# Kernel tuning notes

Measured on AMD Instinct MI355X. Metric: run time of the kernel, lower is better.

Reference implementation:

```python
import jax, jax.numpy as jnp
import numpy as np

TEMPERATURE = 0.07
HARD_K = 10
N, D, NUM_CLASSES = 8192, 256, 128


def setup_inputs() -> dict:
    key = jax.random.key(0)
    kf, kl = jax.random.split(key)
    feats = jax.random.normal(kf, (N, D), dtype=jnp.float32)
    labels = jax.random.randint(kl, (N,), 0, NUM_CLASSES, dtype=jnp.int64)
    return {"feats": feats, "labels": labels}


def _loss(feats, labels):
    n = feats.shape[0]
    # F.normalize(dim=-1) with eps=1e-12
    norm = jnp.maximum(jnp.linalg.norm(feats, axis=-1, keepdims=True), 1e-12)
    z = feats / norm
    sim = (z @ z.T) / TEMPERATURE  # [N, N]

    same = labels[:, None] == labels[None, :]
    eye = jnp.eye(n, dtype=bool)
    same_ns = same & ~eye          # same label, excluding self
    diff = ~same                   # different label

    neg_inf = jnp.float32(-jnp.inf)
    # uniform random positive per row via Gumbel-max over the same-label mask
    g = jax.random.gumbel(jax.random.key(42), (n, n), dtype=jnp.float32)
    pos_idx = jnp.argmax(jnp.where(same_ns, g, neg_inf), axis=1)  # [N]
    pos_logit = jnp.take_along_axis(sim, pos_idx[:, None], axis=1)[:, 0]

    # hard negatives: top-k of sims over different-label columns
    neg_sims = jnp.where(diff, sim, neg_inf)
    hard_vals, _ = jax.lax.top_k(neg_sims, HARD_K)  # [N, K]; exp(-inf)=0 handles rows with <K negatives

    num = jnp.exp(pos_logit)
    den = num + jnp.sum(jnp.exp(hard_vals), axis=1)
    li = -jnp.log(jnp.maximum(num / jnp.maximum(den, 1e-8), 1e-8))

    valid = jnp.any(same_ns, axis=1) & jnp.any(diff, axis=1)
    cnt = jnp.maximum(jnp.sum(valid), 1)
    return jnp.sum(jnp.where(valid, li, 0.0)) / cnt.astype(li.dtype)


def reference(feats, labels):
    return _loss(feats, labels)
```

## Files before the change

### kernel.cpp

```cpp
#include <hip/hip_runtime.h>
#include <cstdint>
#include <math.h>

#define N_     8192
#define D_     256
#define NLBL   128
#define TEMP_INV 14.285714285714286f
#define HARDK  10
#define THETA  0.16f
#define GCAP   256

#define NCHUNK 64
#define CHUNK  (N_ / NCHUNK)
#define TILES  (CHUNK / 32)
#define CSLOT  8
#define NTRI   ((NCHUNK * (NCHUNK + 1)) / 2)

typedef __attribute__((ext_vector_type(8)))  short bf16x8;
typedef __attribute__((ext_vector_type(16))) float f32x16;

__device__ __forceinline__ uint32_t rotl32(uint32_t x, int n) {
  return (x << n) | (x >> (32 - n));
}
__device__ uint32_t tf_bits(uint32_t idx) {
  uint32_t x0 = 0u, x1 = idx;
  const uint32_t k0 = 0u, k1 = 42u;
  const uint32_t k2 = k0 ^ k1 ^ 0x1BD11BDAu;
  x0 += k0; x1 += k1;
#define TFR(r) { x0 += x1; x1 = rotl32(x1, r); x1 ^= x0; }
  TFR(13) TFR(15) TFR(26) TFR(6)
  x0 += k1; x1 += k2 + 1u;
  TFR(17) TFR(29) TFR(16) TFR(24)
  x0 += k2; x1 += k0 + 2u;
  TFR(13) TFR(15) TFR(26) TFR(6)
  x0 += k0; x1 += k1 + 3u;
  TFR(17) TFR(29) TFR(16) TFR(24)
  x0 += k1; x1 += k2 + 4u;
  TFR(13) TFR(15) TFR(26) TFR(6)
  x0 += k2; x1 += k0 + 5u;
#undef TFR
  return x0 ^ x1;
}

__device__ __forceinline__ uint32_t f2bf(float x) {
  uint32_t b = __float_as_uint(x);
  return (b + 0x7FFFu + ((b >> 16) & 1u)) >> 16;
}

__global__ __launch_bounds__(256) void prep_group_kernel(
    const float* __restrict__ feats, const int* __restrict__ labels,
    float* __restrict__ inv_norm, unsigned short* __restrict__ zt,
    uint32_t* __restrict__ mask_g, int* __restrict__ glist, int* __restrict__ cnt_g) {
  __shared__ uint4 tile[16][33];
  __shared__ int lcnt;
  const int tid = threadIdx.x;

  if (blockIdx.x < 512) {
    const int row0 = blockIdx.x * 16;
    const int wv = tid >> 6, l = tid & 63;
#pragma unroll
    for (int rr = 0; rr < 4; ++rr) {
      const int rloc = wv * 4 + rr;
      const int row = row0 + rloc;
      float4 v = ((const float4*)feats)[(size_t)row * 64 + l];
      float ss = v.x * v.x + v.y * v.y + v.z * v.z + v.w * v.w;
#pragma unroll
      for (int o = 32; o; o >>= 1) ss += __shfl_xor(ss, o);
      float inv = 1.0f / fmaxf(sqrtf(ss), 1e-12f);
      if (l == 0) inv_norm[row] = inv;
      uint2 p;
      p.x = f2bf(v.x * inv) | (f2bf(v.y * inv) << 16);
      p.y = f2bf(v.z * inv) | (f2bf(v.w * inv) << 16);
      *(uint2*)((char*)&tile[0][0] + rloc * 528 + l * 8) = p;
    }
    __syncthreads();
#pragma unroll
    for (int it = 0; it < 2; ++it) {
      int idx = it * 256 + tid;
      int c = idx >> 4, r = idx & 15;
      ((uint4*)zt)[(size_t)c * N_ + row0 + r] = tile[r][c];
    }
  } else {
    const int b = blockIdx.x - 512;
    const int lane = tid & 63, wv = tid >> 6;
    if (tid == 0) lcnt = 0;
    __syncthreads();
    for (int it = 0; it < N_; it += 256) {
      int col = it + tid;
      bool pred = (labels[col] == b);
      unsigned long long m = __ballot(pred);
      if (lane == 0) {
        int w0 = (it + wv * 64) >> 5;
        mask_g[b * 256 + w0]     = (uint32_t)m;
        mask_g[b * 256 + w0 + 1] = (uint32_t)(m >> 32);
      }
      if (pred) {
        int p = atomicAdd(&lcnt, 1);
        if (p < GCAP) glist[b * GCAP + p] = col;
      }
    }
    __syncthreads();
    if (tid == 0) cnt_g[b] = lcnt;
  }
}

__device__ __forceinline__ void stage_tile(const unsigned short* zt, char (*AbK)[1024],
                                           int colT, int wid, int l, int kg) {
  const char* base = (const char*)zt + ((size_t)kg * N_ + colT + (l & 31)) * 16;
#pragma unroll
  for (int q = 0; q < 4; ++q) {
    const int kk = wid * 4 + q;
    __builtin_amdgcn_global_load_lds(
        (const __attribute__((address_space(1))) void*)(base + (size_t)kk * (2 * N_ * 16)),
        (__attribute__((address_space(3))) void*)(&AbK[kk][0]), 16, 0, 0);
  }
}

#define INS8(H0,H1,H2,H3,H4,H5,H6,H7,POS,C) \
  { H0 = (POS==0)?(C):H0; H1 = (POS==1)?(C):H1; H2 = (POS==2)?(C):H2; H3 = (POS==3)?(C):H3; \
    H4 = (POS==4)?(C):H4; H5 = (POS==5)?(C):H5; H6 = (POS==6)?(C):H6; H7 = (POS==7)?(C):H7; \
    ++POS; }

__global__ __launch_bounds__(256) void collect_kernel(const unsigned short* __restrict__ zt,
                                                      const int* __restrict__ labels,
                                                      const uint32_t* __restrict__ mask_g,
                                                      float* __restrict__ vals,
                                                      int* __restrict__ counts) {
  __shared__ char Ab[2][16][1024];
  __shared__ float mcell[128 * 8];
  __shared__ int   mcnt[128];

  const int tid = threadIdx.x;
  const int l = tid & 63, wid = tid >> 6;
  const int kg = l >> 5;

  const int bid = (blockIdx.x & 7) * (NTRI / 8) + (blockIdx.x >> 3);

  int rc = 0, rem = bid;
  while (rem >= NCHUNK - rc) { rem -= NCHUNK - rc; ++rc; }
  const int cc = rc + rem;
  const bool offdiag = (cc > rc);

  const int row0 = rc * 128;
  const int col0 = cc * CHUNK;
  const int rowW = row0 + wid * 32 + (l & 31);
  const int lab = labels[rowW];

  if (tid < 128) mcnt[tid] = 0;

  uint32_t mW[TILES];
  {
    uint4 m0 = *(const uint4*)(mask_g + lab * 256 + (col0 >> 5));
    mW[0] = m0.x; mW[1] = m0.y; mW[2] = m0.z; mW[3] = m0.w;
  }

  bf16x8 bf[16];
  {
    const uint4* ztq = (const uint4*)zt;
#pragma unroll
    for (int kk = 0; kk < 16; ++kk)
      bf[kk] = *(const bf16x8*)&ztq[(size_t)(kk * 2 + kg) * N_ + rowW];
  }

  float h0=0,h1=0,h2=0,h3=0,h4=0,h5=0,h6=0,h7=0;
  int pos = 0;
  float* vb = vals + ((size_t)rowW * NCHUNK + cc) * CSLOT;

  stage_tile(zt, Ab[0], col0, wid, l, kg);
  __syncthreads();

  int buf = 0;
#pragma unroll
  for (int t = 0; t < TILES; ++t) {
    if (t + 1 < TILES) stage_tile(zt, Ab[buf ^ 1], col0 + (t + 1) * 32, wid, l, kg);

    f32x16 acc;
#pragma unroll
    for (int r = 0; r < 16; ++r) acc[r] = 0.f;
    __builtin_amdgcn_s_setprio(1);
#pragma unroll
    for (int kk = 0; kk < 16; ++kk) {
      bf16x8 a = *(const bf16x8*)&Ab[buf][kk][l * 16];
      acc = __builtin_amdgcn_mfma_f32_32x32x16_bf16(a, bf[kk], acc, 0, 0, 0);
    }
    __builtin_amdgcn_s_setprio(0);

    const uint32_t wsh = mW[t] >> (kg * 4);
#pragma unroll
    for (int r = 0; r < 16; ++r) {
      const int cpos = (r & 3) + 8 * (r >> 2);
      bool hit = ((((wsh >> cpos) & 1u) == 0u) && (acc[r] > THETA));
      if (__any(hit)) {
        if (hit) {
          INS8(h0,h1,h2,h3,h4,h5,h6,h7, pos, acc[r]);
          if (offdiag) {
            int jc = t * 32 + cpos + 4 * kg;
            int p = atomicAdd(&mcnt[jc], 1);
            if (p < 8) mcell[jc * 8 + p] = acc[r];
          }
        }
      }
    }
    __syncthreads();
    buf ^= 1;
  }

  if (kg == 0) {
    if (pos > 0) vb[0] = h0;  if (pos > 1) vb[1] = h1;
    if (pos > 2) vb[2] = h2;  if (pos > 3) vb[3] = h3;
    if (pos > 4) vb[4] = h4;  if (pos > 5) vb[5] = h5;
    if (pos > 6) vb[6] = h6;  if (pos > 7) vb[7] = h7;
  } else {
    if (pos > 0) vb[7] = h0;  if (pos > 1) vb[6] = h1;
    if (pos > 2) vb[5] = h2;  if (pos > 3) vb[4] = h3;
    if (pos > 4) vb[3] = h4;  if (pos > 5) vb[2] = h5;
    if (pos > 6) vb[1] = h6;  if (pos > 7) vb[0] = h7;
  }
  counts[(rowW * NCHUNK + cc) * 2 + kg] = pos;

  if (offdiag) {
    int jc = tid >> 1, half = tid & 1;
    float4 m = *(float4*)&mcell[jc * 8 + half * 4];
    float* dm = vals + ((size_t)(col0 + jc) * NCHUNK + rc) * CSLOT + half * 4;
    *(float4*)dm = m;
    if (half == 0) {
      counts[((col0 + jc) * NCHUNK + rc) * 2 + 0] = mcnt[jc];
      counts[((col0 + jc) * NCHUNK + rc) * 2 + 1] = 0;
    }
  }
}

__global__ __launch_bounds__(256) void finalize_kernel(
    const float* __restrict__ feats, const int* __restrict__ labels,
    const float* __restrict__ inv_norm,
    const int* __restrict__ glist, const int* __restrict__ cnt_g,
    const int* __restrict__ counts, const float* __restrict__ vals,
    float* __restrict__ li, int* __restrict__ valid) {
  const int row = blockIdx.x * 4 + (threadIdx.x >> 6);
  const int lane = threadIdx.x & 63;
  const int lab = labels[row];
  const int gc = cnt_g[lab];
  const int gn = gc < GCAP ? gc : GCAP;
  const float4* feats4 = (const float4*)feats;

  uint32_t bk = 0u; int bj = -1;
  for (int e = lane; e < gn; e += 64) {
    int j = glist[lab * GCAP + e];
    if (j != row) {
      uint32_t key = tf_bits((uint32_t)row * (uint32_t)N_ + (uint32_t)j) >> 9;
      if (bj < 0 || key > bk || (key == bk && j < bj)) { bk = key; bj = j; }
    }
  }
#pragma unroll
  for (int o = 32; o; o >>= 1) {
    uint32_t ok = __shfl_xor(bk, o);
    int oj = __shfl_xor(bj, o);
    if (oj >= 0 && (bj < 0 || ok > bk || (ok == bk && oj < bj))) { bk = ok; bj = oj; }
  }

  float pc = 0.f;
  if (bj >= 0) {
    float4 a = feats4[(size_t)row * 64 + lane];
    float4 b = feats4[(size_t)bj * 64 + lane];
    float p = a.x * b.x + a.y * b.y + a.z * b.z + a.w * b.w;
#pragma unroll
    for (int o = 32; o; o >>= 1) p += __shfl_xor(p, o);
    pc = p * inv_norm[row] * inv_norm[bj];
  }

  float vv[8];
  int ovf = 0;
#pragma unroll
  for (int q = 0; q < 8; ++q) {
    int s = lane + 64 * q;
    int cell = s >> 3, wi = s & 7;
    int c0 = counts[(row * NCHUNK + cell) * 2 + 0];
    int c1 = counts[(row * NCHUNK + cell) * 2 + 1];
    ovf |= (c0 + c1 > CSLOT) ? 1 : 0;
    float val = vals[(size_t)row * (NCHUNK * CSLOT) + s];
    int c1b = c1 < CSLOT ? c1 : CSLOT;
    bool live = (wi < c0) || (wi >= CSLOT - c1b);
    vv[q] = live ? val : -INFINITY;
  }

  float num = expf(pc * TEMP_INV);
  float den = num;
  int got = 0;
#pragma unroll 1
  for (int it = 0; it < HARDK; ++it) {
    float lm = fmaxf(fmaxf(fmaxf(vv[0], vv[1]), fmaxf(vv[2], vv[3])),
                     fmaxf(fmaxf(vv[4], vv[5]), fmaxf(vv[6], vv[7])));
    float wm = lm;
#pragma unroll
    for (int o = 32; o; o >>= 1) wm = fmaxf(wm, __shfl_xor(wm, o));
    if (wm < -1e37f) break;
    den += expf(wm * TEMP_INV);
    ++got;
    unsigned long long b = __ballot(lm == wm);
    int fl = __ffsll((long long)b) - 1;
    if (lane == fl) {
      if      (vv[0] == wm) vv[0] = -INFINITY;
      else if (vv[1] == wm) vv[1] = -INFINITY;
      else if (vv[2] == wm) vv[2] = -INFINITY;
      else if (vv[3] == wm) vv[3] = -INFINITY;
      else if (vv[4] == wm) vv[4] = -INFINITY;
      else if (vv[5] == wm) vv[5] = -INFINITY;
      else if (vv[6] == wm) vv[6] = -INFINITY;
      else                  vv[7] = -INFINITY;
    }
  }

  const int ndiff = N_ - gc;
  const bool vld = (bj >= 0) && (ndiff > 0);
  const int want = ndiff < HARDK ? ndiff : HARDK;

  if (vld && (__any(ovf) || got < want)) {
    float tk[HARDK];
#pragma unroll
    for (int k = 0; k < HARDK; ++k) tk[k] = -INFINITY;
    const float invr = inv_norm[row];
    const float4 a = feats4[(size_t)row * 64 + lane];
#pragma unroll 1
    for (int j = 0; j < N_; ++j) {
      if (j == row || labels[j] == lab) continue;
      float4 b = feats4[(size_t)j * 64 + lane];
      float p = a.x * b.x + a.y * b.y + a.z * b.z + a.w * b.w;
#pragma unroll
      for (int o = 32; o; o >>= 1) p += __shfl_xor(p, o);
      float c = p * invr * inv_norm[j];
      if (c > tk[0]) {
        tk[0] = c;
#pragma unroll
        for (int q = 0; q < HARDK - 1; ++q)
          if (tk[q] > tk[q + 1]) { float tmp = tk[q]; tk[q] = tk[q + 1]; tk[q + 1] = tmp; }
      }
    }
    den = num;
#pragma unroll
    for (int k = 0; k < HARDK; ++k)
      if (tk[k] > -1e37f) den += expf(tk[k] * TEMP_INV);
  }

  float L = 0.f;
  if (vld) L = -logf(fmaxf(num / fmaxf(den, 1e-8f), 1e-8f));
  if (lane == 0) {
    li[row] = L;
    valid[row] = vld ? 1 : 0;
  }
}

__global__ __launch_bounds__(256) void reduce_kernel(const float* __restrict__ li,
                                                     const int* __restrict__ valid,
                                                     float* __restrict__ out) {
  __shared__ float ssum[4];
  __shared__ int scnt[4];
  float s = 0.f; int c = 0;
  for (int i = threadIdx.x; i < N_; i += 256) { s += li[i]; c += valid[i]; }
#pragma unroll
  for (int o = 32; o; o >>= 1) { s += __shfl_down(s, o); c += __shfl_down(c, o); }
  if ((threadIdx.x & 63) == 0) { ssum[threadIdx.x >> 6] = s; scnt[threadIdx.x >> 6] = c; }
  __syncthreads();
  if (threadIdx.x == 0) {
    float S = 0.f; int C = 0;
    for (int w = 0; w < 4; ++w) { S += ssum[w]; C += scnt[w]; }
    out[0] = S / (float)(C > 0 ? C : 1);
  }
}

extern "C" void kernel_launch(void* const* d_in, const int* in_sizes, int n_in,
                              void* d_out, int out_size, void* d_ws, size_t ws_size,
                              hipStream_t stream) {
  const float* feats  = (const float*)d_in[0];
  const int*   labels = (const int*)d_in[1];
  float* out = (float*)d_out;

  char* w = (char*)d_ws;
  unsigned short* zt  = (unsigned short*)w;  w += (size_t)N_ * D_ * 2;
  float* inv_norm = (float*)w;               w += (size_t)N_ * 4;
  uint32_t* mask_g = (uint32_t*)w;           w += (size_t)NLBL * 256 * 4;
  int* glist = (int*)w;                      w += (size_t)NLBL * GCAP * 4;
  int* cnt_g = (int*)w;                      w += (size_t)NLBL * 4;
  int* counts = (int*)w;                     w += (size_t)N_ * NCHUNK * 2 * 4;
  float* vals = (float*)w;                   w += (size_t)N_ * NCHUNK * CSLOT * 4;
  float* li_arr = (float*)w;                 w += (size_t)N_ * 4;
  int* valid_arr = (int*)w;                  w += (size_t)N_ * 4;

  hipLaunchKernelGGL(prep_group_kernel, dim3(640), dim3(256), 0, stream,
                     feats, labels, inv_norm, zt, mask_g, glist, cnt_g);
  hipLaunchKernelGGL(collect_kernel, dim3(NTRI), dim3(256), 0, stream,
                     zt, labels, mask_g, vals, counts);
  hipLaunchKernelGGL(finalize_kernel, dim3(N_ / 4), dim3(256), 0, stream,
                     feats, labels, inv_norm, glist, cnt_g, counts, vals, li_arr, valid_arr);
  hipLaunchKernelGGL(reduce_kernel, dim3(1), dim3(256), 0, stream, li_arr, valid_arr, out);
}
```

Before: 83.16 us.

## Split collect tiles into K-halves and rebuild label grouping with atomics

The collect kernel now stages and multiplies each 32-column tile in two K-halves, which halves the LDS double buffer to 16 KB and is meant to let more blocks fit per CU. The label-grouping blocks in prep are also redesigned. Instead of 128 blocks each scanning all 8192 labels, 32 blocks each handle 256 columns, building mask words with LDS atomicOr and counts with global atomicAdd, after a memset of cnt_g. The catch is that glist order becomes nondeterministic, and the half-tiles add a sync per half.

```diff
diff --git a/kernel.cpp b/kernel.cpp
--- a/kernel.cpp
+++ b/kernel.cpp
@@ -13,6 +13,7 @@
 #define NCHUNK 64
 #define CHUNK  (N_ / NCHUNK)
 #define TILES  (CHUNK / 32)
+#define HALVES (TILES * 2)
 #define CSLOT  8
 #define NTRI   ((NCHUNK * (NCHUNK + 1)) / 2)
 
@@ -51,11 +52,10 @@
     const float* __restrict__ feats, const int* __restrict__ labels,
     float* __restrict__ inv_norm, unsigned short* __restrict__ zt,
     uint32_t* __restrict__ mask_g, int* __restrict__ glist, int* __restrict__ cnt_g) {
-  __shared__ uint4 tile[16][33];
-  __shared__ int lcnt;
   const int tid = threadIdx.x;
 
   if (blockIdx.x < 512) {
+    __shared__ uint4 tile[16][33];
     const int row0 = blockIdx.x * 16;
     const int wv = tid >> 6, l = tid & 63;
 #pragma unroll
@@ -81,38 +81,37 @@
       ((uint4*)zt)[(size_t)c * N_ + row0 + r] = tile[r][c];
     }
   } else {
+    __shared__ uint32_t mlds[NLBL * 8];
     const int b = blockIdx.x - 512;
-    const int lane = tid & 63, wv = tid >> 6;
-    if (tid == 0) lcnt = 0;
+    const int c0 = b * 256;
+#pragma unroll
+    for (int it = 0; it < 4; ++it) mlds[it * 256 + tid] = 0u;
     __syncthreads();
-    for (int it = 0; it < N_; it += 256) {
-      int col = it + tid;
-      bool pred = (labels[col] == b);
-      unsigned long long m = __ballot(pred);
-      if (lane == 0) {
-        int w0 = (it + wv * 64) >> 5;
-        mask_g[b * 256 + w0]     = (uint32_t)m;
-        mask_g[b * 256 + w0 + 1] = (uint32_t)(m >> 32);
-      }
-      if (pred) {
-        int p = atomicAdd(&lcnt, 1);
-        if (p < GCAP) glist[b * GCAP + p] = col;
-      }
-    }
+    const int col = c0 + tid;
+    const int lab = labels[col];
+    atomicOr(&mlds[lab * 8 + ((col & 255) >> 5)], 1u << (col & 31));
+    int p = atomicAdd(&cnt_g[lab], 1);
+    if (p < GCAP) glist[lab * GCAP + p] = col;
     __syncthreads();
-    if (tid == 0) cnt_g[b] = lcnt;
-  }
-}
-
-__device__ __forceinline__ void stage_tile(const unsigned short* zt, char (*AbK)[1024],
-                                           int colT, int wid, int l, int kg) {
+#pragma unroll
+    for (int it = 0; it < 4; ++it) {
+      int idx = it * 256 + tid;
+      int lb = idx >> 3, wd = idx & 7;
+      mask_g[lb * 256 + (c0 >> 5) + wd] = mlds[idx];
+    }
+  }
+}
+
+__device__ __forceinline__ void stage_half(const unsigned short* zt, char (*AbK)[1024],
+                                           int colT, int kh, int wid, int l, int kg) {
   const char* base = (const char*)zt + ((size_t)kg * N_ + colT + (l & 31)) * 16;
 #pragma unroll
-  for (int q = 0; q < 4; ++q) {
-    const int kk = wid * 4 + q;
+  for (int q = 0; q < 2; ++q) {
+    const int kkloc = wid * 2 + q;
+    const int kk = kh * 8 + kkloc;
     __builtin_amdgcn_global_load_lds(
         (const __attribute__((address_space(1))) void*)(base + (size_t)kk * (2 * N_ * 16)),
-        (__attribute__((address_space(3))) void*)(&AbK[kk][0]), 16, 0, 0);
+        (__attribute__((address_space(3))) void*)(&AbK[kkloc][0]), 16, 0, 0);
   }
 }
 
@@ -126,7 +125,7 @@
                                                       const uint32_t* __restrict__ mask_g,
                                                       float* __restrict__ vals,
                                                       int* __restrict__ counts) {
-  __shared__ char Ab[2][16][1024];
+  __shared__ char Ab[2][8][1024];
   __shared__ float mcell[128 * 8];
   __shared__ int   mcnt[128];
 
@@ -166,37 +165,43 @@
   int pos = 0;
   float* vb = vals + ((size_t)rowW * NCHUNK + cc) * CSLOT;
 
-  stage_tile(zt, Ab[0], col0, wid, l, kg);
+  stage_half(zt, Ab[0], col0, 0, wid, l, kg);
   __syncthreads();
 
+  f32x16 acc;
   int buf = 0;
 #pragma unroll
-  for (int t = 0; t < TILES; ++t) {
-    if (t + 1 < TILES) stage_tile(zt, Ab[buf ^ 1], col0 + (t + 1) * 32, wid, l, kg);
-
-    f32x16 acc;
-#pragma unroll
-    for (int r = 0; r < 16; ++r) acc[r] = 0.f;
+  for (int h = 0; h < HALVES; ++h) {
+    const int t = h >> 1, kh = h & 1;
+    if (h + 1 < HALVES)
+      stage_half(zt, Ab[buf ^ 1], col0 + ((h + 1) >> 1) * 32, (h + 1) & 1, wid, l, kg);
+
+    if (kh == 0) {
+#pragma unroll
+      for (int r = 0; r < 16; ++r) acc[r] = 0.f;
+    }
     __builtin_amdgcn_s_setprio(1);
 #pragma unroll
-    for (int kk = 0; kk < 16; ++kk) {
-      bf16x8 a = *(const bf16x8*)&Ab[buf][kk][l * 16];
-      acc = __builtin_amdgcn_mfma_f32_32x32x16_bf16(a, bf[kk], acc, 0, 0, 0);
+    for (int kkloc = 0; kkloc < 8; ++kkloc) {
+      bf16x8 a = *(const bf16x8*)&Ab[buf][kkloc][l * 16];
+      acc = __builtin_amdgcn_mfma_f32_32x32x16_bf16(a, bf[kh * 8 + kkloc], acc, 0, 0, 0);
     }
     __builtin_amdgcn_s_setprio(0);
 
-    const uint32_t wsh = mW[t] >> (kg * 4);
-#pragma unroll
-    for (int r = 0; r < 16; ++r) {
-      const int cpos = (r & 3) + 8 * (r >> 2);
-      bool hit = ((((wsh >> cpos) & 1u) == 0u) && (acc[r] > THETA));
-      if (__any(hit)) {
-        if (hit) {
-          INS8(h0,h1,h2,h3,h4,h5,h6,h7, pos, acc[r]);
-          if (offdiag) {
-            int jc = t * 32 + cpos + 4 * kg;
-            int p = atomicAdd(&mcnt[jc], 1);
-            if (p < 8) mcell[jc * 8 + p] = acc[r];
+    if (kh == 1) {
+      const uint32_t wsh = mW[t] >> (kg * 4);
+#pragma unroll
+      for (int r = 0; r < 16; ++r) {
+        const int cpos = (r & 3) + 8 * (r >> 2);
+        bool hit = ((((wsh >> cpos) & 1u) == 0u) && (acc[r] > THETA));
+        if (__any(hit)) {
+          if (hit) {
+            INS8(h0,h1,h2,h3,h4,h5,h6,h7, pos, acc[r]);
+            if (offdiag) {
+              int jc = t * 32 + cpos + 4 * kg;
+              int p = atomicAdd(&mcnt[jc], 1);
+              if (p < 8) mcell[jc * 8 + p] = acc[r];
+            }
           }
         }
       }
@@ -385,7 +390,8 @@
   float* li_arr = (float*)w;                 w += (size_t)N_ * 4;
   int* valid_arr = (int*)w;                  w += (size_t)N_ * 4;
 
-  hipLaunchKernelGGL(prep_group_kernel, dim3(640), dim3(256), 0, stream,
+  hipMemsetAsync(cnt_g, 0, NLBL * sizeof(int), stream);
+  hipLaunchKernelGGL(prep_group_kernel, dim3(544), dim3(256), 0, stream,
                      feats, labels, inv_norm, zt, mask_g, glist, cnt_g);
   hipLaunchKernelGGL(collect_kernel, dim3(NTRI), dim3(256), 0, stream,
                      zt, labels, mask_g, vals, counts);
```

Measured after the change: 87.97 us. +5.8%, slower.
